# Optimization experiments

Measured on AMD Instinct MI355X. Metric: run time of the kernel, lower is better.

Reference implementation:

```python
import jax, jax.numpy as jnp
import numpy as np

N = 4096       # number of graph nodes
F_IN = 512     # in_features == out_features (residual connection requires it)
H = 8          # n_heads


def setup_inputs() -> dict:
    key = jax.random.key(0)
    k1, k2, k3, k4, k5 = jax.random.split(key, 5)
    s = 1.0 / np.sqrt(F_IN)  # keep projections well-scaled
    x = jax.random.normal(k1, (N, F_IN), dtype=jnp.float32)
    Wq = jax.random.normal(k2, (F_IN, F_IN), dtype=jnp.float32) * s
    Wk = jax.random.normal(k3, (F_IN, F_IN), dtype=jnp.float32) * s
    Wv = jax.random.normal(k4, (F_IN, F_IN), dtype=jnp.float32) * s
    adj = jax.random.randint(k5, (H, N, N), 0, 2, dtype=jnp.int32)
    return {"x": x, "Wq": Wq, "Wk": Wk, "Wv": Wv, "adj": adj}


def reference(x, Wq, Wk, Wv, adj):
    # Faithful to torch GraphAttentionLayer.forward (eval mode, dropout off).
    # NOTE: the torch code builds keys = input.repeat(N,1,1).detach() -> the
    # K/V inputs are stop-gradient copies of x; projections are per-node, so
    # we compute them once instead of materializing the redundant [N,N,F].
    n, f = x.shape
    d = f // H  # head dim (chunk_size)
    xk = jax.lax.stop_gradient(x)
    # nn.Linear: y = x @ W.T ; split feature dim into heads -> [H, N, d]
    Q = (x @ Wq.T).reshape(n, H, d).transpose(1, 0, 2)
    K = (xk @ Wk.T).reshape(n, H, d).transpose(1, 0, 2)
    V = (xk @ Wv.T).reshape(n, H, d).transpose(1, 0, 2)
    # scaled by sqrt(in_features) (NOT head dim), as in the original
    scores = jnp.einsum('hnd,hmd->hnm', Q, K) / jnp.sqrt(jnp.float32(f))
    scores = jnp.where(adj > 0, scores, jnp.float32(-9e15))
    attn = jax.nn.softmax(scores, axis=-1)          # [H, N, N]
    out = jnp.einsum('hnm,hmd->hnd', attn, V)       # [H, N, d]
    out = out.transpose(1, 0, 2).reshape(n, f)      # concat heads -> [N, F]
    return jax.nn.elu(out + x)[:, None, :]          # [N, 1, F] like torch
```

## Files before the change

### kernel.cpp

```cpp
#include <hip/hip_runtime.h>
#include <hip/hip_bf16.h>

#define NN 4096
#define FF 512
#define NH 8
#define DH 64

typedef __attribute__((ext_vector_type(8))) short bf16x8;
typedef __attribute__((ext_vector_type(4))) float f32x4;

#define X_OFF  0
#define W_OFF  2097152
#define QF_OFF 2883584
#define KF_OFF 4980736
#define VF_OFF 7077888
#define PACC_OFF 9175040
#define PDEN_USHORT_OFF 17563648

__device__ __forceinline__ ushort f2bf(float f) {
    __hip_bfloat16 h = __float2bfloat16(f);
    return __builtin_bit_cast(ushort, h);
}
__device__ __forceinline__ float bf2f(ushort u) {
    unsigned int v = ((unsigned int)u) << 16;
    return __builtin_bit_cast(float, v);
}

__global__ __launch_bounds__(256) void cvt_kernel(const float* __restrict__ x,
                                                  const float* __restrict__ wq,
                                                  const float* __restrict__ wk,
                                                  const float* __restrict__ wv,
                                                  ushort* __restrict__ ws) {
    int i = blockIdx.x * 256 + threadIdx.x;
    int base = i * 4;
    const float* src;
    int off;
    float sc = 1.f;
    if (base < 2097152) { src = x; off = base; }
    else {
        int t = base - 2097152;
        int m = t >> 18;
        src = (m == 0) ? wq : ((m == 1) ? wk : wv);
        if (m == 0) sc = 0.044194173824159216f;
        off = t & 262143;
    }
    float4 v = *reinterpret_cast<const float4*>(src + off);
    ushort4 o;
    o.x = f2bf(v.x * sc); o.y = f2bf(v.y * sc); o.z = f2bf(v.z * sc); o.w = f2bf(v.w * sc);
    *reinterpret_cast<ushort4*>(ws + base) = o;
}

__global__ __launch_bounds__(256) void qkv_kernel(ushort* __restrict__ ws) {
    int bx = blockIdx.x;
    int mat = bx >> 3;
    int fb  = bx & 7;
    int mb  = blockIdx.y;
    int wave = threadIdx.x >> 6, lane = threadIdx.x & 63;
    int la = lane & 15, lk = lane >> 4;

    int m_base = mb * 64 + wave * 16;
    int f_base = fb * 64;

    const ushort* xb = ws + X_OFF;
    const ushort* wb = ws + W_OFF + mat * 262144;

    f32x4 acc[4];
#pragma unroll
    for (int t = 0; t < 4; ++t) acc[t] = (f32x4){0.f, 0.f, 0.f, 0.f};

#pragma unroll 4
    for (int k0 = 0; k0 < 512; k0 += 32) {
        bf16x8 a = *reinterpret_cast<const bf16x8*>(xb + (size_t)(m_base + la) * 512 + k0 + lk * 8);
#pragma unroll
        for (int ft = 0; ft < 4; ++ft) {
            bf16x8 b = *reinterpret_cast<const bf16x8*>(wb + (size_t)(f_base + ft * 16 + la) * 512 + k0 + lk * 8);
            acc[ft] = __builtin_amdgcn_mfma_f32_16x16x32_bf16(a, b, acc[ft], 0, 0, 0);
        }
    }

#pragma unroll
    for (int ft = 0; ft < 4; ++ft) {
#pragma unroll
        for (int r = 0; r < 4; ++r) {
            int n = m_base + lk * 4 + r;
            int d = ft * 16 + la;
            ushort v = f2bf(acc[ft][r]);
            if (mat < 2) {
                ushort* base = ws + (mat == 0 ? QF_OFF : KF_OFF) + (size_t)fb * 262144;
                int blk = n >> 4, rr = n & 15;
                int half = d >> 5, lkk = (d >> 3) & 3, e = d & 7;
                base[(((size_t)blk * 2 + half) * 64 + lkk * 16 + rr) * 8 + e] = v;
            } else {
                ushort* base = ws + VF_OFF + (size_t)fb * 262144;
                int kb64 = n >> 6, kc = n & 63;
                int hf = kc >> 5, lkv = (kc >> 3) & 3, ev = kc & 7;
                int dt = d >> 4, lav = d & 15;
                base[((((size_t)kb64 * 4 + dt) * 2 + hf) * 64 + lkv * 16 + lav) * 8 + ev] = v;
            }
        }
    }
}

__global__ __launch_bounds__(256, 4) void attn_kernel(const int* __restrict__ adj,
                                                      const ushort* __restrict__ ws,
                                                      ushort* __restrict__ pacc,
                                                      float* __restrict__ pden) {
    __shared__ ushort P[4][16][72];

    int bid = blockIdx.x;
    int h = bid & 7, qb = (bid >> 3) & 63, ks = bid >> 9;
    int wave = threadIdx.x >> 6, lane = threadIdx.x & 63;
    int la = lane & 15, lk = lane >> 4;
    int q0w = qb * 64 + wave * 16;

    const ushort* Qh = ws + QF_OFF + (size_t)h * 262144;
    const ushort* Kh = ws + KF_OFF + (size_t)h * 262144;
    const ushort* Vh = ws + VF_OFF + (size_t)h * 262144;
    const int* adjw = adj + (size_t)h * 16777216 + (size_t)q0w * 4096;

    bf16x8 qa0 = *reinterpret_cast<const bf16x8*>(Qh + ((((size_t)(q0w >> 4)) * 2 + 0) * 64 + lane) * 8);
    bf16x8 qa1 = *reinterpret_cast<const bf16x8*>(Qh + ((((size_t)(q0w >> 4)) * 2 + 1) * 64 + lane) * 8);

    f32x4 acc[4];
    float den[4];
#pragma unroll
    for (int r = 0; r < 4; ++r) {
        acc[r] = (f32x4){0.f, 0.f, 0.f, 0.f};
        den[r] = 0.f;
    }

    const f32x4 zero = {0.f, 0.f, 0.f, 0.f};
    int kbase = ks * 16;

    int adjv[16];
#pragma unroll
    for (int j = 0; j < 16; ++j)
        adjv[j] = __builtin_nontemporal_load(adjw + (size_t)j * 4096 + kbase * 64 + lane);

    for (int it = 0; it < 16; ++it) {
        int kb = kbase + it;

        unsigned long long m[16];
#pragma unroll
        for (int j = 0; j < 16; ++j)
            m[j] = __ballot(adjv[j] != 0);

        unsigned int sel_lo[4], sel_hi[4];
#pragma unroll
        for (int r = 0; r < 4; ++r) {
            unsigned int l0 = (unsigned int)m[r],       h0 = (unsigned int)(m[r] >> 32);
            unsigned int l1 = (unsigned int)m[4 + r],   h1 = (unsigned int)(m[4 + r] >> 32);
            unsigned int l2 = (unsigned int)m[8 + r],   h2 = (unsigned int)(m[8 + r] >> 32);
            unsigned int l3 = (unsigned int)m[12 + r],  h3 = (unsigned int)(m[12 + r] >> 32);
            unsigned int a = (lk & 1) ? l1 : l0, b = (lk & 1) ? l3 : l2;
            sel_lo[r] = (lk & 2) ? b : a;
            unsigned int c = (lk & 1) ? h1 : h0, d = (lk & 1) ? h3 : h2;
            sel_hi[r] = (lk & 2) ? d : c;
        }

        bf16x8 kf[4][2];
#pragma unroll
        for (int kt = 0; kt < 4; ++kt) {
            const ushort* kp = Kh + (((size_t)(kb * 4 + kt) * 2) * 64 + lane) * 8;
            kf[kt][0] = *reinterpret_cast<const bf16x8*>(kp);
            kf[kt][1] = *reinterpret_cast<const bf16x8*>(kp + 512);
        }
        f32x4 s[4];
#pragma unroll
        for (int kt = 0; kt < 4; ++kt) {
            s[kt] = __builtin_amdgcn_mfma_f32_16x16x32_bf16(qa0, kf[kt][0], zero, 0, 0, 0);
            s[kt] = __builtin_amdgcn_mfma_f32_16x16x32_bf16(qa1, kf[kt][1], s[kt], 0, 0, 0);
        }

        bf16x8 vb[4][2];
#pragma unroll
        for (int dt = 0; dt < 4; ++dt) {
            const ushort* vp = Vh + ((((size_t)kb * 4 + dt) * 2) * 64 + lane) * 8;
            vb[dt][0] = *reinterpret_cast<const bf16x8*>(vp);
            vb[dt][1] = *reinterpret_cast<const bf16x8*>(vp + 512);
        }

        int kbn = (it + 1 < 16) ? kb + 1 : kbase;
#pragma unroll
        for (int j = 0; j < 16; ++j)
            adjv[j] = __builtin_nontemporal_load(adjw + (size_t)j * 4096 + kbn * 64 + lane);

#pragma unroll
        for (int r = 0; r < 4; ++r) {
#pragma unroll
            for (int kt = 0; kt < 4; ++kt) {
                unsigned int dw = (kt < 2) ? sel_lo[r] : sel_hi[r];
                unsigned int bit = (dw >> (la + ((kt & 1) << 4))) & 1u;
                float sv = bit ? s[kt][r] : -1e30f;
                float e = __expf(sv);
                den[r] += e;
                P[wave][lk * 4 + r][kt * 16 + la] = f2bf(e);
            }
        }

        bf16x8 pa0 = *reinterpret_cast<const bf16x8*>(&P[wave][la][lk * 8]);
        bf16x8 pa1 = *reinterpret_cast<const bf16x8*>(&P[wave][la][32 + lk * 8]);
#pragma unroll
        for (int dt = 0; dt < 4; ++dt) {
            acc[dt] = __builtin_amdgcn_mfma_f32_16x16x32_bf16(pa0, vb[dt][0], acc[dt], 0, 0, 0);
            acc[dt] = __builtin_amdgcn_mfma_f32_16x16x32_bf16(pa1, vb[dt][1], acc[dt], 0, 0, 0);
        }
    }

#pragma unroll
    for (int r = 0; r < 4; ++r)
#pragma unroll
        for (int mm = 1; mm < 16; mm <<= 1)
            den[r] += __shfl_xor(den[r], mm, 64);

    ushort* pa_out = pacc + ((size_t)ks * 8 + h) * 4096 * 64;
#pragma unroll
    for (int dt = 0; dt < 4; ++dt)
#pragma unroll
        for (int r = 0; r < 4; ++r) {
            int q = q0w + lk * 4 + r;
            __builtin_nontemporal_store(f2bf(acc[dt][r]), pa_out + (size_t)q * 64 + dt * 16 + la);
        }
    if (la == 0) {
        float* pd = pden + ((size_t)ks * 8 + h) * 4096;
#pragma unroll
        for (int r = 0; r < 4; ++r)
            pd[q0w + lk * 4 + r] = den[r];
    }
}

__global__ __launch_bounds__(256) void combine_kernel(const float* __restrict__ x,
                                                      const ushort* __restrict__ pacc,
                                                      const float* __restrict__ pden,
                                                      float* __restrict__ out) {
    int idx = blockIdx.x * 256 + threadIdx.x;
    int n = idx >> 7, fq = idx & 127;
    int h = fq >> 4;
    int d4 = (fq & 15) * 4;

    float4 o = make_float4(0.f, 0.f, 0.f, 0.f);
    float den = 0.f;
#pragma unroll
    for (int ksp = 0; ksp < 4; ++ksp) {
        const ushort* pa = pacc + (((size_t)ksp * 8 + h) * 4096 + n) * 64 + d4;
        ushort4 p = *reinterpret_cast<const ushort4*>(pa);
        o.x += bf2f(p.x); o.y += bf2f(p.y); o.z += bf2f(p.z); o.w += bf2f(p.w);
        den += pden[((size_t)ksp * 8 + h) * 4096 + n];
    }
    float4 xv = *reinterpret_cast<const float4*>(x + (size_t)n * 512 + fq * 4);
    float inv = 1.f / den;
    float4 r;
    r.x = o.x * inv + xv.x;
    r.y = o.y * inv + xv.y;
    r.z = o.z * inv + xv.z;
    r.w = o.w * inv + xv.w;
    r.x = (r.x > 0.f) ? r.x : (__expf(r.x) - 1.f);
    r.y = (r.y > 0.f) ? r.y : (__expf(r.y) - 1.f);
    r.z = (r.z > 0.f) ? r.z : (__expf(r.z) - 1.f);
    r.w = (r.w > 0.f) ? r.w : (__expf(r.w) - 1.f);
    *reinterpret_cast<float4*>(out + (size_t)n * 512 + fq * 4) = r;
}

extern "C" void kernel_launch(void* const* d_in, const int* in_sizes, int n_in,
                              void* d_out, int out_size, void* d_ws, size_t ws_size,
                              hipStream_t stream) {
    const float* x  = (const float*)d_in[0];
    const float* wq = (const float*)d_in[1];
    const float* wk = (const float*)d_in[2];
    const float* wv = (const float*)d_in[3];
    const int*   adj = (const int*)d_in[4];
    float* out = (float*)d_out;
    ushort* ws = (ushort*)d_ws;
    ushort* pacc = ws + PACC_OFF;
    float* pden = (float*)(ws + PDEN_USHORT_OFF);

    cvt_kernel<<<2816, 256, 0, stream>>>(x, wq, wk, wv, ws);
    qkv_kernel<<<dim3(24, 64), 256, 0, stream>>>(ws);
    attn_kernel<<<2048, 256, 0, stream>>>(adj, ws, pacc, pden);
    combine_kernel<<<2048, 256, 0, stream>>>(x, pacc, pden, out);
}
```

Before: 243.9 us.

## Stage K/V tiles into double-buffered LDS and load adjacency in MFMA layout

Each block now cooperatively copies K and V tiles for the next key block into double-buffered shared memory with global_load_lds, instead of every wave loading them redundantly from global memory. The adjacency is loaded directly in the MFMA accumulator layout, so the ballot and bit-select mask building is replaced by an additive float mask. The adjacency prefetch for the last iteration is also skipped. This adds a __syncthreads per iteration and more LDS, and lowers the launch-bounds occupancy hint from 4 to 3 blocks. The new adjacency loads are 16-wide per row rather than 64-wide, so coalescing of the dominant int32 adj stream may get worse.

```diff
diff --git a/kernel.cpp b/kernel.cpp
--- a/kernel.cpp
+++ b/kernel.cpp
@@ -101,10 +101,30 @@
     }
 }
 
-__global__ __launch_bounds__(256, 4) void attn_kernel(const int* __restrict__ adj,
+
+#define STAGE(BUF, KB)                                                                     \
+    {                                                                                      \
+        const ushort* sbase_ = (wave < 2) ? Kh : Vh;                                       \
+        ushort(*dbuf_)[512] = (wave < 2) ? kbuf[BUF] : vbuf[BUF];                          \
+        int t0_ = (wave & 1) * 4;                                                          \
+        _Pragma("unroll")                                                                  \
+        for (int t_ = 0; t_ < 4; ++t_) {                                                   \
+            int tile_ = t0_ + t_;                                                          \
+            const ushort* src_ = sbase_ +                                                  \
+                (((size_t)(KB) * 4 + (tile_ >> 1)) * 2 + (tile_ & 1)) * 512 + lane * 8;    \
+            __builtin_amdgcn_global_load_lds(                                              \
+                (const __attribute__((address_space(1))) unsigned int*)src_,               \
+                (__attribute__((address_space(3))) unsigned int*)&dbuf_[tile_][0],         \
+                16, 0, 0);                                                                 \
+        }                                                                                  \
+    }
+
+__global__ __launch_bounds__(256, 3) void attn_kernel(const int* __restrict__ adj,
                                                       const ushort* __restrict__ ws,
                                                       ushort* __restrict__ pacc,
                                                       float* __restrict__ pden) {
+    __shared__ ushort kbuf[2][8][512];
+    __shared__ ushort vbuf[2][8][512];
     __shared__ ushort P[4][16][72];
 
     int bid = blockIdx.x;
@@ -132,79 +152,65 @@
     const f32x4 zero = {0.f, 0.f, 0.f, 0.f};
     int kbase = ks * 16;
 
+    STAGE(0, kbase)
     int adjv[16];
 #pragma unroll
-    for (int j = 0; j < 16; ++j)
-        adjv[j] = __builtin_nontemporal_load(adjw + (size_t)j * 4096 + kbase * 64 + lane);
+    for (int kt = 0; kt < 4; ++kt)
+#pragma unroll
+        for (int r = 0; r < 4; ++r)
+            adjv[kt * 4 + r] = __builtin_nontemporal_load(
+                adjw + (size_t)(lk * 4 + r) * 4096 + (size_t)kbase * 64 + kt * 16 + la);
+    __syncthreads();
 
     for (int it = 0; it < 16; ++it) {
         int kb = kbase + it;
-
-        unsigned long long m[16];
+        int cur = it & 1;
+
+        if (it < 15) STAGE(cur ^ 1, kb + 1)
+
+        float fmask[16];
 #pragma unroll
         for (int j = 0; j < 16; ++j)
-            m[j] = __ballot(adjv[j] != 0);
-
-        unsigned int sel_lo[4], sel_hi[4];
-#pragma unroll
-        for (int r = 0; r < 4; ++r) {
-            unsigned int l0 = (unsigned int)m[r],       h0 = (unsigned int)(m[r] >> 32);
-            unsigned int l1 = (unsigned int)m[4 + r],   h1 = (unsigned int)(m[4 + r] >> 32);
-            unsigned int l2 = (unsigned int)m[8 + r],   h2 = (unsigned int)(m[8 + r] >> 32);
-            unsigned int l3 = (unsigned int)m[12 + r],  h3 = (unsigned int)(m[12 + r] >> 32);
-            unsigned int a = (lk & 1) ? l1 : l0, b = (lk & 1) ? l3 : l2;
-            sel_lo[r] = (lk & 2) ? b : a;
-            unsigned int c = (lk & 1) ? h1 : h0, d = (lk & 1) ? h3 : h2;
-            sel_hi[r] = (lk & 2) ? d : c;
-        }
-
-        bf16x8 kf[4][2];
+            fmask[j] = adjv[j] ? 0.f : -1e30f;
+
+        if (it < 15) {
+#pragma unroll
+            for (int kt = 0; kt < 4; ++kt)
+#pragma unroll
+                for (int r = 0; r < 4; ++r)
+                    adjv[kt * 4 + r] = __builtin_nontemporal_load(
+                        adjw + (size_t)(lk * 4 + r) * 4096 + (size_t)(kb + 1) * 64 + kt * 16 + la);
+        }
+
+        f32x4 s[4];
 #pragma unroll
         for (int kt = 0; kt < 4; ++kt) {
-            const ushort* kp = Kh + (((size_t)(kb * 4 + kt) * 2) * 64 + lane) * 8;
-            kf[kt][0] = *reinterpret_cast<const bf16x8*>(kp);
-            kf[kt][1] = *reinterpret_cast<const bf16x8*>(kp + 512);
-        }
-        f32x4 s[4];
-#pragma unroll
-        for (int kt = 0; kt < 4; ++kt) {
-            s[kt] = __builtin_amdgcn_mfma_f32_16x16x32_bf16(qa0, kf[kt][0], zero, 0, 0, 0);
-            s[kt] = __builtin_amdgcn_mfma_f32_16x16x32_bf16(qa1, kf[kt][1], s[kt], 0, 0, 0);
-        }
-
-        bf16x8 vb[4][2];
-#pragma unroll
-        for (int dt = 0; dt < 4; ++dt) {
-            const ushort* vp = Vh + ((((size_t)kb * 4 + dt) * 2) * 64 + lane) * 8;
-            vb[dt][0] = *reinterpret_cast<const bf16x8*>(vp);
-            vb[dt][1] = *reinterpret_cast<const bf16x8*>(vp + 512);
-        }
-
-        int kbn = (it + 1 < 16) ? kb + 1 : kbase;
-#pragma unroll
-        for (int j = 0; j < 16; ++j)
-            adjv[j] = __builtin_nontemporal_load(adjw + (size_t)j * 4096 + kbn * 64 + lane);
-
-#pragma unroll
-        for (int r = 0; r < 4; ++r) {
-#pragma unroll
-            for (int kt = 0; kt < 4; ++kt) {
-                unsigned int dw = (kt < 2) ? sel_lo[r] : sel_hi[r];
-                unsigned int bit = (dw >> (la + ((kt & 1) << 4))) & 1u;
-                float sv = bit ? s[kt][r] : -1e30f;
-                float e = __expf(sv);
+            bf16x8 kf0 = *reinterpret_cast<const bf16x8*>(&kbuf[cur][kt * 2 + 0][lane * 8]);
+            bf16x8 kf1 = *reinterpret_cast<const bf16x8*>(&kbuf[cur][kt * 2 + 1][lane * 8]);
+            s[kt] = __builtin_amdgcn_mfma_f32_16x16x32_bf16(qa0, kf0, zero, 0, 0, 0);
+            s[kt] = __builtin_amdgcn_mfma_f32_16x16x32_bf16(qa1, kf1, s[kt], 0, 0, 0);
+        }
+
+#pragma unroll
+        for (int kt = 0; kt < 4; ++kt)
+#pragma unroll
+            for (int r = 0; r < 4; ++r) {
+                float e = __expf(s[kt][r] + fmask[kt * 4 + r]);
                 den[r] += e;
                 P[wave][lk * 4 + r][kt * 16 + la] = f2bf(e);
             }
-        }
 
         bf16x8 pa0 = *reinterpret_cast<const bf16x8*>(&P[wave][la][lk * 8]);
         bf16x8 pa1 = *reinterpret_cast<const bf16x8*>(&P[wave][la][32 + lk * 8]);
 #pragma unroll
         for (int dt = 0; dt < 4; ++dt) {
-            acc[dt] = __builtin_amdgcn_mfma_f32_16x16x32_bf16(pa0, vb[dt][0], acc[dt], 0, 0, 0);
-            acc[dt] = __builtin_amdgcn_mfma_f32_16x16x32_bf16(pa1, vb[dt][1], acc[dt], 0, 0, 0);
-        }
+            bf16x8 vb0 = *reinterpret_cast<const bf16x8*>(&vbuf[cur][dt * 2 + 0][lane * 8]);
+            bf16x8 vb1 = *reinterpret_cast<const bf16x8*>(&vbuf[cur][dt * 2 + 1][lane * 8]);
+            acc[dt] = __builtin_amdgcn_mfma_f32_16x16x32_bf16(pa0, vb0, acc[dt], 0, 0, 0);
+            acc[dt] = __builtin_amdgcn_mfma_f32_16x16x32_bf16(pa1, vb1, acc[dt], 0, 0, 0);
+        }
+
+        __syncthreads();
     }
 
 #pragma unroll
```

After: 222.7 us. 1.1x faster.

## Pre-pack adjacency into bitmasks in a fused pack+QKV kernel

Applied to the files above, without the earlier changes.

Adds a pass that reads the int32 adjacency once and writes one bit per entry, packed by ballot, and fuses it into the QKV projection kernel as extra blocks. The attention kernel then loads two 32-bit mask words per row per key block instead of streaming int32 adjacency and running ballots and selects in its inner loop. K and V loads are also moved next to their MFMA uses, which lowers register pressure. The adjacency stream is still read in full, now in a separate pass, plus a small extra bitmask write and read.

```diff
diff --git a/kernel.cpp b/kernel.cpp
--- a/kernel.cpp
+++ b/kernel.cpp
@@ -16,6 +16,7 @@
 #define VF_OFF 7077888
 #define PACC_OFF 9175040
 #define PDEN_USHORT_OFF 17563648
+#define PK_USHORT_OFF 17825792
 
 __device__ __forceinline__ ushort f2bf(float f) {
     __hip_bfloat16 h = __float2bfloat16(f);
@@ -50,12 +51,40 @@
     *reinterpret_cast<ushort4*>(ws + base) = o;
 }
 
-__global__ __launch_bounds__(256) void qkv_kernel(ushort* __restrict__ ws) {
-    int bx = blockIdx.x;
-    int mat = bx >> 3;
-    int fb  = bx & 7;
-    int mb  = blockIdx.y;
+__global__ __launch_bounds__(256) void packqkv_kernel(const int* __restrict__ adj,
+                                                      unsigned int* __restrict__ pk,
+                                                      ushort* __restrict__ ws) {
+    int bid = blockIdx.x;
     int wave = threadIdx.x >> 6, lane = threadIdx.x & 63;
+
+    if (bid < 8192) {
+        int row = bid * 4 + wave;
+        const int* ar = adj + (size_t)row * 4096;
+        unsigned long long* outp = reinterpret_cast<unsigned long long*>(pk + (size_t)row * 128);
+        for (int it = 0; it < 64; it += 4) {
+            int v0 = __builtin_nontemporal_load(ar + (it + 0) * 64 + lane);
+            int v1 = __builtin_nontemporal_load(ar + (it + 1) * 64 + lane);
+            int v2 = __builtin_nontemporal_load(ar + (it + 2) * 64 + lane);
+            int v3 = __builtin_nontemporal_load(ar + (it + 3) * 64 + lane);
+            unsigned long long b0 = __ballot(v0 != 0);
+            unsigned long long b1 = __ballot(v1 != 0);
+            unsigned long long b2 = __ballot(v2 != 0);
+            unsigned long long b3 = __ballot(v3 != 0);
+            if (lane == 0) {
+                outp[it + 0] = b0;
+                outp[it + 1] = b1;
+                outp[it + 2] = b2;
+                outp[it + 3] = b3;
+            }
+        }
+        return;
+    }
+
+    int q = bid - 8192;
+    int mat = q >> 9;
+    int rem = q & 511;
+    int fb = rem & 7;
+    int mb = rem >> 3;
     int la = lane & 15, lk = lane >> 4;
 
     int m_base = mb * 64 + wave * 16;
@@ -101,7 +130,7 @@
     }
 }
 
-__global__ __launch_bounds__(256, 4) void attn_kernel(const int* __restrict__ adj,
+__global__ __launch_bounds__(256, 4) void attn_kernel(const unsigned int* __restrict__ pk,
                                                       const ushort* __restrict__ ws,
                                                       ushort* __restrict__ pacc,
                                                       float* __restrict__ pden) {
@@ -116,82 +145,49 @@
     const ushort* Qh = ws + QF_OFF + (size_t)h * 262144;
     const ushort* Kh = ws + KF_OFF + (size_t)h * 262144;
     const ushort* Vh = ws + VF_OFF + (size_t)h * 262144;
-    const int* adjw = adj + (size_t)h * 16777216 + (size_t)q0w * 4096;
+    const unsigned int* pkh = pk + (size_t)h * 4096 * 128;
 
     bf16x8 qa0 = *reinterpret_cast<const bf16x8*>(Qh + ((((size_t)(q0w >> 4)) * 2 + 0) * 64 + lane) * 8);
     bf16x8 qa1 = *reinterpret_cast<const bf16x8*>(Qh + ((((size_t)(q0w >> 4)) * 2 + 1) * 64 + lane) * 8);
 
     f32x4 acc[4];
     float den[4];
+    int rowm[4];
 #pragma unroll
     for (int r = 0; r < 4; ++r) {
         acc[r] = (f32x4){0.f, 0.f, 0.f, 0.f};
         den[r] = 0.f;
+        rowm[r] = (q0w + lk * 4 + r) * 128;
     }
 
     const f32x4 zero = {0.f, 0.f, 0.f, 0.f};
-    int kbase = ks * 16;
-
-    int adjv[16];
-#pragma unroll
-    for (int j = 0; j < 16; ++j)
-        adjv[j] = __builtin_nontemporal_load(adjw + (size_t)j * 4096 + kbase * 64 + lane);
+    int kb0 = ks * 16;
 
     for (int it = 0; it < 16; ++it) {
-        int kb = kbase + it;
-
-        unsigned long long m[16];
-#pragma unroll
-        for (int j = 0; j < 16; ++j)
-            m[j] = __ballot(adjv[j] != 0);
-
-        unsigned int sel_lo[4], sel_hi[4];
-#pragma unroll
-        for (int r = 0; r < 4; ++r) {
-            unsigned int l0 = (unsigned int)m[r],       h0 = (unsigned int)(m[r] >> 32);
-            unsigned int l1 = (unsigned int)m[4 + r],   h1 = (unsigned int)(m[4 + r] >> 32);
-            unsigned int l2 = (unsigned int)m[8 + r],   h2 = (unsigned int)(m[8 + r] >> 32);
-            unsigned int l3 = (unsigned int)m[12 + r],  h3 = (unsigned int)(m[12 + r] >> 32);
-            unsigned int a = (lk & 1) ? l1 : l0, b = (lk & 1) ? l3 : l2;
-            sel_lo[r] = (lk & 2) ? b : a;
-            unsigned int c = (lk & 1) ? h1 : h0, d = (lk & 1) ? h3 : h2;
-            sel_hi[r] = (lk & 2) ? d : c;
-        }
-
-        bf16x8 kf[4][2];
+        int kb = kb0 + it;
+
+        uint2 mk[4];
+#pragma unroll
+        for (int r = 0; r < 4; ++r)
+            mk[r] = *reinterpret_cast<const uint2*>(pkh + rowm[r] + kb * 2);
+
+        f32x4 s[4];
 #pragma unroll
         for (int kt = 0; kt < 4; ++kt) {
             const ushort* kp = Kh + (((size_t)(kb * 4 + kt) * 2) * 64 + lane) * 8;
-            kf[kt][0] = *reinterpret_cast<const bf16x8*>(kp);
-            kf[kt][1] = *reinterpret_cast<const bf16x8*>(kp + 512);
-        }
-        f32x4 s[4];
+            bf16x8 kf0 = *reinterpret_cast<const bf16x8*>(kp);
+            bf16x8 kf1 = *reinterpret_cast<const bf16x8*>(kp + 512);
+            s[kt] = __builtin_amdgcn_mfma_f32_16x16x32_bf16(qa0, kf0, zero, 0, 0, 0);
+            s[kt] = __builtin_amdgcn_mfma_f32_16x16x32_bf16(qa1, kf1, s[kt], 0, 0, 0);
+        }
+
 #pragma unroll
         for (int kt = 0; kt < 4; ++kt) {
-            s[kt] = __builtin_amdgcn_mfma_f32_16x16x32_bf16(qa0, kf[kt][0], zero, 0, 0, 0);
-            s[kt] = __builtin_amdgcn_mfma_f32_16x16x32_bf16(qa1, kf[kt][1], s[kt], 0, 0, 0);
-        }
-
-        bf16x8 vb[4][2];
-#pragma unroll
-        for (int dt = 0; dt < 4; ++dt) {
-            const ushort* vp = Vh + ((((size_t)kb * 4 + dt) * 2) * 64 + lane) * 8;
-            vb[dt][0] = *reinterpret_cast<const bf16x8*>(vp);
-            vb[dt][1] = *reinterpret_cast<const bf16x8*>(vp + 512);
-        }
-
-        int kbn = (it + 1 < 16) ? kb + 1 : kbase;
-#pragma unroll
-        for (int j = 0; j < 16; ++j)
-            adjv[j] = __builtin_nontemporal_load(adjw + (size_t)j * 4096 + kbn * 64 + lane);
-
-#pragma unroll
-        for (int r = 0; r < 4; ++r) {
-#pragma unroll
-            for (int kt = 0; kt < 4; ++kt) {
-                unsigned int dw = (kt < 2) ? sel_lo[r] : sel_hi[r];
-                unsigned int bit = (dw >> (la + ((kt & 1) << 4))) & 1u;
-                float sv = bit ? s[kt][r] : -1e30f;
+            int sh = la + ((kt & 1) << 4);
+#pragma unroll
+            for (int r = 0; r < 4; ++r) {
+                unsigned int dw = (kt < 2) ? mk[r].x : mk[r].y;
+                float sv = ((dw >> sh) & 1u) ? s[kt][r] : -1e30f;
                 float e = __expf(sv);
                 den[r] += e;
                 P[wave][lk * 4 + r][kt * 16 + la] = f2bf(e);
@@ -202,8 +198,11 @@
         bf16x8 pa1 = *reinterpret_cast<const bf16x8*>(&P[wave][la][32 + lk * 8]);
 #pragma unroll
         for (int dt = 0; dt < 4; ++dt) {
-            acc[dt] = __builtin_amdgcn_mfma_f32_16x16x32_bf16(pa0, vb[dt][0], acc[dt], 0, 0, 0);
-            acc[dt] = __builtin_amdgcn_mfma_f32_16x16x32_bf16(pa1, vb[dt][1], acc[dt], 0, 0, 0);
+            const ushort* vp = Vh + ((((size_t)kb * 4 + dt) * 2) * 64 + lane) * 8;
+            bf16x8 vb0 = *reinterpret_cast<const bf16x8*>(vp);
+            bf16x8 vb1 = *reinterpret_cast<const bf16x8*>(vp + 512);
+            acc[dt] = __builtin_amdgcn_mfma_f32_16x16x32_bf16(pa0, vb0, acc[dt], 0, 0, 0);
+            acc[dt] = __builtin_amdgcn_mfma_f32_16x16x32_bf16(pa1, vb1, acc[dt], 0, 0, 0);
         }
     }
 
@@ -218,8 +217,8 @@
     for (int dt = 0; dt < 4; ++dt)
 #pragma unroll
         for (int r = 0; r < 4; ++r) {
-            int q = q0w + lk * 4 + r;
-            __builtin_nontemporal_store(f2bf(acc[dt][r]), pa_out + (size_t)q * 64 + dt * 16 + la);
+            int qi = q0w + lk * 4 + r;
+            __builtin_nontemporal_store(f2bf(acc[dt][r]), pa_out + (size_t)qi * 64 + dt * 16 + la);
         }
     if (la == 0) {
         float* pd = pden + ((size_t)ks * 8 + h) * 4096;
@@ -273,9 +272,10 @@
     ushort* ws = (ushort*)d_ws;
     ushort* pacc = ws + PACC_OFF;
     float* pden = (float*)(ws + PDEN_USHORT_OFF);
+    unsigned int* pk = (unsigned int*)(ws + PK_USHORT_OFF);
 
     cvt_kernel<<<2816, 256, 0, stream>>>(x, wq, wk, wv, ws);
-    qkv_kernel<<<dim3(24, 64), 256, 0, stream>>>(ws);
-    attn_kernel<<<2048, 256, 0, stream>>>(adj, ws, pacc, pden);
+    packqkv_kernel<<<9728, 256, 0, stream>>>(adj, pk, ws);
+    attn_kernel<<<2048, 256, 0, stream>>>(pk, ws, pacc, pden);
     combine_kernel<<<2048, 256, 0, stream>>>(x, pacc, pden, out);
 }
```

After: 250.0 us. 2.5% more time.

## Transpose QK^T MFMA so each lane owns one query row, simplify masking

Applied to the files above, without the earlier changes.

Swaps the MFMA operand order so the score tile is transposed: each lane now holds four consecutive keys for a single query row. This lets the adjacency bitmask be selected once per lane by a butterfly over la, lets P be written as packed ushort4 to LDS, and keeps a single denominator per lane that needs only two shuffles. The change also interleaves the K/V loads with the MFMAs instead of holding full register arrays, adds sched_barriers around an adjacency prefetch that skips the last iteration, and lowers launch_bounds occupancy from 4 to 3. Fewer VALU select and shuffle ops are the goal; the risk is lower occupancy and less latency hiding for the K/V loads.

```diff
diff --git a/kernel.cpp b/kernel.cpp
--- a/kernel.cpp
+++ b/kernel.cpp
@@ -101,7 +101,7 @@
     }
 }
 
-__global__ __launch_bounds__(256, 4) void attn_kernel(const int* __restrict__ adj,
+__global__ __launch_bounds__(256, 3) void attn_kernel(const int* __restrict__ adj,
                                                       const ushort* __restrict__ ws,
                                                       ushort* __restrict__ pacc,
                                                       float* __restrict__ pden) {
@@ -122,110 +122,91 @@
     bf16x8 qa1 = *reinterpret_cast<const bf16x8*>(Qh + ((((size_t)(q0w >> 4)) * 2 + 1) * 64 + lane) * 8);
 
     f32x4 acc[4];
-    float den[4];
-#pragma unroll
-    for (int r = 0; r < 4; ++r) {
-        acc[r] = (f32x4){0.f, 0.f, 0.f, 0.f};
-        den[r] = 0.f;
-    }
+#pragma unroll
+    for (int r = 0; r < 4; ++r) acc[r] = (f32x4){0.f, 0.f, 0.f, 0.f};
+    float den = 0.f;
+    int lk4 = lk * 4;
 
     const f32x4 zero = {0.f, 0.f, 0.f, 0.f};
-    int kbase = ks * 16;
+    int kb0 = ks * 16;
 
     int adjv[16];
 #pragma unroll
     for (int j = 0; j < 16; ++j)
-        adjv[j] = __builtin_nontemporal_load(adjw + (size_t)j * 4096 + kbase * 64 + lane);
+        adjv[j] = __builtin_nontemporal_load(adjw + (size_t)j * 4096 + (size_t)kb0 * 64 + lane);
 
     for (int it = 0; it < 16; ++it) {
-        int kb = kbase + it;
-
-        unsigned long long m[16];
+        int kb = kb0 + it;
+
+        unsigned long long mm[16];
 #pragma unroll
         for (int j = 0; j < 16; ++j)
-            m[j] = __ballot(adjv[j] != 0);
-
-        unsigned int sel_lo[4], sel_hi[4];
-#pragma unroll
-        for (int r = 0; r < 4; ++r) {
-            unsigned int l0 = (unsigned int)m[r],       h0 = (unsigned int)(m[r] >> 32);
-            unsigned int l1 = (unsigned int)m[4 + r],   h1 = (unsigned int)(m[4 + r] >> 32);
-            unsigned int l2 = (unsigned int)m[8 + r],   h2 = (unsigned int)(m[8 + r] >> 32);
-            unsigned int l3 = (unsigned int)m[12 + r],  h3 = (unsigned int)(m[12 + r] >> 32);
-            unsigned int a = (lk & 1) ? l1 : l0, b = (lk & 1) ? l3 : l2;
-            sel_lo[r] = (lk & 2) ? b : a;
-            unsigned int c = (lk & 1) ? h1 : h0, d = (lk & 1) ? h3 : h2;
-            sel_hi[r] = (lk & 2) ? d : c;
-        }
-
-        bf16x8 kf[4][2];
+            mm[j] = __ballot(adjv[j] != 0);
+
+        unsigned long long t8[8], t4[4], t2[2], msel;
+#pragma unroll
+        for (int i = 0; i < 8; ++i) t8[i] = (la & 1) ? mm[2 * i + 1] : mm[2 * i];
+#pragma unroll
+        for (int i = 0; i < 4; ++i) t4[i] = (la & 2) ? t8[2 * i + 1] : t8[2 * i];
+#pragma unroll
+        for (int i = 0; i < 2; ++i) t2[i] = (la & 4) ? t4[2 * i + 1] : t4[2 * i];
+        msel = (la & 8) ? t2[1] : t2[0];
+        unsigned int mlo = (unsigned int)msel;
+        unsigned int mhi = (unsigned int)(msel >> 32);
+        __builtin_amdgcn_sched_barrier(0);
+
+        if (it < 15) {
+#pragma unroll
+            for (int j = 0; j < 16; ++j)
+                adjv[j] = __builtin_nontemporal_load(adjw + (size_t)j * 4096 + (size_t)(kb + 1) * 64 + lane);
+        }
+        __builtin_amdgcn_sched_barrier(0);
+
 #pragma unroll
         for (int kt = 0; kt < 4; ++kt) {
             const ushort* kp = Kh + (((size_t)(kb * 4 + kt) * 2) * 64 + lane) * 8;
-            kf[kt][0] = *reinterpret_cast<const bf16x8*>(kp);
-            kf[kt][1] = *reinterpret_cast<const bf16x8*>(kp + 512);
-        }
-        f32x4 s[4];
-#pragma unroll
-        for (int kt = 0; kt < 4; ++kt) {
-            s[kt] = __builtin_amdgcn_mfma_f32_16x16x32_bf16(qa0, kf[kt][0], zero, 0, 0, 0);
-            s[kt] = __builtin_amdgcn_mfma_f32_16x16x32_bf16(qa1, kf[kt][1], s[kt], 0, 0, 0);
-        }
-
-        bf16x8 vb[4][2];
+            bf16x8 kf0 = *reinterpret_cast<const bf16x8*>(kp);
+            bf16x8 kf1 = *reinterpret_cast<const bf16x8*>(kp + 512);
+            f32x4 s = __builtin_amdgcn_mfma_f32_16x16x32_bf16(kf0, qa0, zero, 0, 0, 0);
+            s = __builtin_amdgcn_mfma_f32_16x16x32_bf16(kf1, qa1, s, 0, 0, 0);
+            unsigned int dw = (kt < 2) ? mlo : mhi;
+            int sh = ((kt & 1) << 4) + lk4;
+            ushort4 pw;
+            float e0 = __expf(((dw >> (sh + 0)) & 1u) ? s[0] : -1e30f);
+            float e1 = __expf(((dw >> (sh + 1)) & 1u) ? s[1] : -1e30f);
+            float e2 = __expf(((dw >> (sh + 2)) & 1u) ? s[2] : -1e30f);
+            float e3 = __expf(((dw >> (sh + 3)) & 1u) ? s[3] : -1e30f);
+            den += (e0 + e1) + (e2 + e3);
+            pw.x = f2bf(e0); pw.y = f2bf(e1); pw.z = f2bf(e2); pw.w = f2bf(e3);
+            *reinterpret_cast<ushort4*>(&P[wave][la][kt * 16 + lk4]) = pw;
+        }
+
+        bf16x8 pa0 = *reinterpret_cast<const bf16x8*>(&P[wave][la][lk * 8]);
+        bf16x8 pa1 = *reinterpret_cast<const bf16x8*>(&P[wave][la][32 + lk * 8]);
 #pragma unroll
         for (int dt = 0; dt < 4; ++dt) {
             const ushort* vp = Vh + ((((size_t)kb * 4 + dt) * 2) * 64 + lane) * 8;
-            vb[dt][0] = *reinterpret_cast<const bf16x8*>(vp);
-            vb[dt][1] = *reinterpret_cast<const bf16x8*>(vp + 512);
-        }
-
-        int kbn = (it + 1 < 16) ? kb + 1 : kbase;
-#pragma unroll
-        for (int j = 0; j < 16; ++j)
-            adjv[j] = __builtin_nontemporal_load(adjw + (size_t)j * 4096 + kbn * 64 + lane);
-
+            bf16x8 vb0 = *reinterpret_cast<const bf16x8*>(vp);
+            bf16x8 vb1 = *reinterpret_cast<const bf16x8*>(vp + 512);
+            acc[dt] = __builtin_amdgcn_mfma_f32_16x16x32_bf16(pa0, vb0, acc[dt], 0, 0, 0);
+            acc[dt] = __builtin_amdgcn_mfma_f32_16x16x32_bf16(pa1, vb1, acc[dt], 0, 0, 0);
+        }
+    }
+
+    den += __shfl_xor(den, 16, 64);
+    den += __shfl_xor(den, 32, 64);
+
+    ushort* pa_out = pacc + ((size_t)ks * 8 + h) * 4096 * 64;
+#pragma unroll
+    for (int dt = 0; dt < 4; ++dt)
 #pragma unroll
         for (int r = 0; r < 4; ++r) {
-#pragma unroll
-            for (int kt = 0; kt < 4; ++kt) {
-                unsigned int dw = (kt < 2) ? sel_lo[r] : sel_hi[r];
-                unsigned int bit = (dw >> (la + ((kt & 1) << 4))) & 1u;
-                float sv = bit ? s[kt][r] : -1e30f;
-                float e = __expf(sv);
-                den[r] += e;
-                P[wave][lk * 4 + r][kt * 16 + la] = f2bf(e);
-            }
-        }
-
-        bf16x8 pa0 = *reinterpret_cast<const bf16x8*>(&P[wave][la][lk * 8]);
-        bf16x8 pa1 = *reinterpret_cast<const bf16x8*>(&P[wave][la][32 + lk * 8]);
-#pragma unroll
-        for (int dt = 0; dt < 4; ++dt) {
-            acc[dt] = __builtin_amdgcn_mfma_f32_16x16x32_bf16(pa0, vb[dt][0], acc[dt], 0, 0, 0);
-            acc[dt] = __builtin_amdgcn_mfma_f32_16x16x32_bf16(pa1, vb[dt][1], acc[dt], 0, 0, 0);
-        }
-    }
-
-#pragma unroll
-    for (int r = 0; r < 4; ++r)
-#pragma unroll
-        for (int mm = 1; mm < 16; mm <<= 1)
-            den[r] += __shfl_xor(den[r], mm, 64);
-
-    ushort* pa_out = pacc + ((size_t)ks * 8 + h) * 4096 * 64;
-#pragma unroll
-    for (int dt = 0; dt < 4; ++dt)
-#pragma unroll
-        for (int r = 0; r < 4; ++r) {
-            int q = q0w + lk * 4 + r;
-            __builtin_nontemporal_store(f2bf(acc[dt][r]), pa_out + (size_t)q * 64 + dt * 16 + la);
-        }
-    if (la == 0) {
+            int qi = q0w + lk4 + r;
+            __builtin_nontemporal_store(f2bf(acc[dt][r]), pa_out + (size_t)qi * 64 + dt * 16 + la);
+        }
+    if (lane < 16) {
         float* pd = pden + ((size_t)ks * 8 + h) * 4096;
-#pragma unroll
-        for (int r = 0; r < 4; ++r)
-            pd[q0w + lk * 4 + r] = den[r];
+        pd[q0w + lane] = den;
     }
 }
 
```

New measurement: 670.7 us. +175.0%, slower.
